# Kernel optimization log

Measured on AMD Instinct MI355X. Metric: run time of the kernel, lower is better.

The kernel has to match this reference:

```python
import jax, jax.numpy as jnp
import numpy as np

N_NODES = 100000
N_EDGES = 1600000
F_IN = 512
HEADS = 8
C1 = 8            # hidden per head in conv1
N_CLASSES = 40
NEG_SLOPE = 0.2
EPS = 1e-16


def setup_inputs() -> dict:
    key = jax.random.key(0)
    ks = jax.random.split(key, 12)
    x = jax.random.normal(ks[0], (N_NODES, F_IN), dtype=jnp.float32)
    # edges with src != dst (PyG SuperGAT removes then re-adds self-loops)
    src = jax.random.randint(ks[1], (N_EDGES,), 0, N_NODES)
    off = jax.random.randint(ks[2], (N_EDGES,), 1, N_NODES)
    dst = (src + off) % N_NODES
    edge_index = jnp.stack([src, dst]).astype(jnp.int64)
    def glorot(k, shape):
        fan = shape[0] + shape[-1]
        return jax.random.uniform(k, shape, jnp.float32, -1.0, 1.0) * np.sqrt(6.0 / fan)
    W1 = glorot(ks[3], (F_IN, HEADS * C1))
    att_l1 = glorot(ks[4], (HEADS, C1))
    att_r1 = glorot(ks[5], (HEADS, C1))
    b1 = jnp.zeros((HEADS * C1,), jnp.float32)
    W2 = glorot(ks[6], (HEADS * C1, HEADS * N_CLASSES))
    att_l2 = glorot(ks[7], (HEADS, N_CLASSES))
    att_r2 = glorot(ks[8], (HEADS, N_CLASSES))
    b2 = jnp.zeros((N_CLASSES,), jnp.float32)
    return {"x": x, "edge_index": edge_index, "W1": W1, "att_l1": att_l1,
            "att_r1": att_r1, "b1": b1, "W2": W2, "att_l2": att_l2,
            "att_r2": att_r2, "b2": b2}


def supergat_conv(x, edge_index, W, att_l, att_r, bias, concat):
    """SuperGATConv with attention_type='MX', eval mode (no dropout)."""
    N = x.shape[0]
    H, C = att_l.shape
    xw = (x @ W).reshape(N, H, C)
    loops = jnp.arange(N)
    src = jnp.concatenate([edge_index[0], loops])  # j (source)
    dst = jnp.concatenate([edge_index[1], loops])  # i (target)
    x_j = xw[src]                                   # [E,H,C]
    x_i = xw[dst]                                   # [E,H,C]
    # MX attention: GO score gated by sigmoid of DP logits
    logits = jnp.einsum('ehc,ehc->eh', x_i, x_j)
    alpha = jnp.einsum('ehc,hc->eh', x_j, att_l) + jnp.einsum('ehc,hc->eh', x_i, att_r)
    alpha = alpha * jax.nn.sigmoid(logits)
    alpha = jax.nn.leaky_relu(alpha, NEG_SLOPE)
    # segment softmax over incoming edges of each destination node
    amax = jax.ops.segment_max(alpha, dst, num_segments=N)
    e = jnp.exp(alpha - amax[dst])
    denom = jax.ops.segment_sum(e, dst, num_segments=N)
    a = e / (denom[dst] + EPS)
    out = jax.ops.segment_sum(x_j * a[..., None], dst, num_segments=N)  # [N,H,C]
    out = out.reshape(N, H * C) if concat else out.mean(axis=1)
    return out + bias


def reference(x, edge_index, W1, att_l1, att_r1, b1, W2, att_l2, att_r2, b2):
    # eval mode: F.dropout(p=0.6) is identity, att_loss is 0
    h = jax.nn.elu(supergat_conv(x, edge_index, W1, att_l1, att_r1, b1, concat=True))
    out = supergat_conv(h, edge_index, W2, att_l2, att_r2, b2, concat=False)
    att_loss = jnp.float32(0.0)
    return jax.nn.log_softmax(out, axis=-1), att_loss
```

## Files before the change

### kernel.cpp

```cpp
#include <hip/hip_runtime.h>
#include <cstdint>

#define N_NODES 100000
#define N_EDGES 1600000
#define SCAN_NB 196

typedef short bf16x8 __attribute__((ext_vector_type(8)));
typedef float f32x4 __attribute__((ext_vector_type(4)));
typedef float f32x2 __attribute__((ext_vector_type(2)));

__device__ __forceinline__ uint16_t f2bf(float f) {
    uint32_t b = __float_as_uint(f);
    return (uint16_t)((b + 0x7fffu + ((b >> 16) & 1u)) >> 16);
}
__device__ __forceinline__ float bfval(uint16_t u) {
    return __uint_as_float(((uint32_t)u) << 16);
}
__device__ __forceinline__ float blo(uint32_t u) { return __uint_as_float(u << 16); }
__device__ __forceinline__ float bhi(uint32_t u) { return __uint_as_float(u & 0xffff0000u); }

__device__ __forceinline__ float fast_rcp(float x) { return __builtin_amdgcn_rcpf(x); }

__global__ void cvt_w1(const float* __restrict__ W1, uint16_t* __restrict__ whi,
                       uint16_t* __restrict__ wlo) {
    int gid = blockIdx.x * 256 + threadIdx.x;
    int c = gid & 63, kg = gid >> 6;
    uint32_t dh[4], dl[4];
    #pragma unroll
    for (int t = 0; t < 4; ++t) {
        float v0 = W1[(kg * 8 + 2 * t) * 64 + c];
        float v1 = W1[(kg * 8 + 2 * t + 1) * 64 + c];
        uint16_t h0 = f2bf(v0), h1 = f2bf(v1);
        uint16_t l0 = f2bf(v0 - bfval(h0)), l1 = f2bf(v1 - bfval(h1));
        dh[t] = h0 | ((uint32_t)h1 << 16);
        dl[t] = l0 | ((uint32_t)l1 << 16);
    }
    *(uint4*)(whi + (long)c * 512 + kg * 8) = make_uint4(dh[0], dh[1], dh[2], dh[3]);
    *(uint4*)(wlo + (long)c * 512 + kg * 8) = make_uint4(dl[0], dl[1], dl[2], dl[3]);
}

__global__ __launch_bounds__(256) void wvec_k(const float* __restrict__ W2,
        const float* __restrict__ attl, const float* __restrict__ attr,
        float* __restrict__ wl2, float* __restrict__ wr2) {
    int t = blockIdx.x * 256 + threadIdx.x;
    if (t >= 512) return;
    int h = t >> 6, k = t & 63;
    float sl = 0.f, sr = 0.f;
    #pragma unroll 8
    for (int c = 0; c < 40; ++c) {
        float w = W2[k * 320 + h * 40 + c];
        sl += w * attl[h * 40 + c];
        sr += w * attr[h * 40 + c];
    }
    wl2[t] = sl; wr2[t] = sr;
}

__global__ __launch_bounds__(512) void mcat_k(const float* __restrict__ W2,
        uint16_t* __restrict__ mhi, uint16_t* __restrict__ mlo) {
    __shared__ float Wh[64 * 40];
    int h = blockIdx.x;
    int tid = threadIdx.x;
    for (int t = tid; t < 2560; t += 512) {
        int k = t / 40, c = t % 40;
        Wh[k * 40 + c] = W2[k * 320 + h * 40 + c];
    }
    __syncthreads();
    #pragma unroll
    for (int r = 0; r < 8; ++r) {
        int o = r * 512 + tid;
        int kp = o >> 6, k = o & 63;
        float s = 0.f;
        #pragma unroll 8
        for (int c = 0; c < 40; ++c) s += Wh[k * 40 + c] * Wh[kp * 40 + c];
        uint16_t hi = f2bf(s);
        uint16_t lo = f2bf(s - bfval(hi));
        mhi[(h * 64 + kp) * 64 + k] = hi;
        mlo[(h * 64 + kp) * 64 + k] = lo;
    }
}

__global__ __launch_bounds__(256) void w2z_k(const float* __restrict__ W2,
        uint16_t* __restrict__ w2z) {
    int t = blockIdx.x * 256 + threadIdx.x;
    if (t >= 24576) return;
    int c = t >> 9, kap = t & 511;
    int h = kap >> 6, k = kap & 63;
    float v = (c < 40) ? W2[k * 320 + h * 40 + c] : 0.f;
    w2z[c * 512 + kap] = f2bf(v);
}

__global__ __launch_bounds__(512) void gemm1_mfma(const float* __restrict__ x,
        const uint16_t* __restrict__ w1hi, const uint16_t* __restrict__ w1lo,
        float* __restrict__ xw1, uint16_t* __restrict__ xw1b) {
    __shared__ __align__(16) char Ah[128 * 144];
    __shared__ __align__(16) char Al[128 * 144];
    __shared__ __align__(16) char Bh[64 * 144];
    __shared__ __align__(16) char Bl[64 * 144];
    int tid = threadIdx.x;
    int l = tid & 63, w = tid >> 6;
    long base = (long)blockIdx.x * 128;
    f32x4 acc[4];
    #pragma unroll
    for (int ct = 0; ct < 4; ++ct)
        #pragma unroll
        for (int j = 0; j < 4; ++j) acc[ct][j] = 0.f;

    for (int kb = 0; kb < 512; kb += 64) {
        __syncthreads();
        #pragma unroll
        for (int it = 0; it < 2; ++it) {
            int idx = tid + it * 512;
            int row = idx >> 3, kc = idx & 7;
            long r = base + row; if (r >= N_NODES) r = N_NODES - 1;
            const float4* p = (const float4*)(x + r * 512 + kb + kc * 8);
            float4 f0 = p[0], f1 = p[1];
            float v[8] = {f0.x, f0.y, f0.z, f0.w, f1.x, f1.y, f1.z, f1.w};
            uint32_t dh[4], dl[4];
            #pragma unroll
            for (int t = 0; t < 4; ++t) {
                uint16_t h0 = f2bf(v[2 * t]),     h1 = f2bf(v[2 * t + 1]);
                uint16_t l0 = f2bf(v[2 * t] - bfval(h0));
                uint16_t l1 = f2bf(v[2 * t + 1] - bfval(h1));
                dh[t] = h0 | ((uint32_t)h1 << 16);
                dl[t] = l0 | ((uint32_t)l1 << 16);
            }
            *(uint4*)(Ah + row * 144 + kc * 16) = make_uint4(dh[0], dh[1], dh[2], dh[3]);
            *(uint4*)(Al + row * 144 + kc * 16) = make_uint4(dl[0], dl[1], dl[2], dl[3]);
        }
        {
            int c = tid >> 3, kc = tid & 7;
            *(uint4*)(Bh + c * 144 + kc * 16) =
                *(const uint4*)(w1hi + (long)c * 512 + kb + kc * 8);
            *(uint4*)(Bl + c * 144 + kc * 16) =
                *(const uint4*)(w1lo + (long)c * 512 + kb + kc * 8);
        }
        __syncthreads();
        #pragma unroll
        for (int kk = 0; kk < 2; ++kk) {
            int aoff = (w * 16 + (l & 15)) * 144 + kk * 64 + (l >> 4) * 16;
            bf16x8 ah = *(const bf16x8*)(Ah + aoff);
            bf16x8 alo = *(const bf16x8*)(Al + aoff);
            #pragma unroll
            for (int ct = 0; ct < 4; ++ct) {
                int boff = (ct * 16 + (l & 15)) * 144 + kk * 64 + (l >> 4) * 16;
                bf16x8 bh = *(const bf16x8*)(Bh + boff);
                bf16x8 bl = *(const bf16x8*)(Bl + boff);
                acc[ct] = __builtin_amdgcn_mfma_f32_16x16x32_bf16(ah, bh, acc[ct], 0, 0, 0);
                acc[ct] = __builtin_amdgcn_mfma_f32_16x16x32_bf16(alo, bh, acc[ct], 0, 0, 0);
                acc[ct] = __builtin_amdgcn_mfma_f32_16x16x32_bf16(ah, bl, acc[ct], 0, 0, 0);
            }
        }
    }
    int nrow = w * 16 + (l >> 4) * 4;
    #pragma unroll
    for (int ct = 0; ct < 4; ++ct)
        #pragma unroll
        for (int j = 0; j < 4; ++j) {
            long node = base + nrow + j;
            if (node < N_NODES) {
                int col = ct * 16 + (l & 15);
                xw1[node * 64 + col] = acc[ct][j];
                xw1b[node * 64 + col] = f2bf(acc[ct][j]);
            }
        }
}

__global__ __launch_bounds__(512) void ygemm_mfma(const uint16_t* __restrict__ hjb,
        const uint16_t* __restrict__ mhi, const uint16_t* __restrict__ mlo,
        uint16_t* __restrict__ Y16) {
    __shared__ __align__(16) char Bh[256 * 144];
    __shared__ __align__(16) char Bl[256 * 144];
    int tid = threadIdx.x;
    int l = tid & 63, w = tid >> 6;
    int half = blockIdx.x & 1;
    long base = (long)(blockIdx.x >> 1) * 128;
    #pragma unroll
    for (int it = 0; it < 4; ++it) {
        int idx = tid + it * 512;
        int c = idx >> 3, kc = idx & 7;
        *(uint4*)(Bh + c * 144 + kc * 16) =
            *(const uint4*)(mhi + (long)(half * 256 + c) * 64 + kc * 8);
        *(uint4*)(Bl + c * 144 + kc * 16) =
            *(const uint4*)(mlo + (long)(half * 256 + c) * 64 + kc * 8);
    }
    long n0 = base + w * 16 + (l & 15);
    long nld = n0 < N_NODES ? n0 : N_NODES - 1;
    bf16x8 a[2];
    #pragma unroll
    for (int kk = 0; kk < 2; ++kk)
        a[kk] = *(const bf16x8*)(hjb + nld * 64 + kk * 32 + (l >> 4) * 8);
    __syncthreads();
    f32x4 acc[16];
    #pragma unroll
    for (int ct = 0; ct < 16; ++ct)
        #pragma unroll
        for (int j = 0; j < 4; ++j) acc[ct][j] = 0.f;
    #pragma unroll
    for (int ct = 0; ct < 16; ++ct) {
        #pragma unroll
        for (int kk = 0; kk < 2; ++kk) {
            bf16x8 bh = *(const bf16x8*)(Bh + (ct * 16 + (l & 15)) * 144 + kk * 64 + (l >> 4) * 16);
            bf16x8 bl = *(const bf16x8*)(Bl + (ct * 16 + (l & 15)) * 144 + kk * 64 + (l >> 4) * 16);
            acc[ct] = __builtin_amdgcn_mfma_f32_16x16x32_bf16(bh, a[kk], acc[ct], 0, 0, 0);
            acc[ct] = __builtin_amdgcn_mfma_f32_16x16x32_bf16(bl, a[kk], acc[ct], 0, 0, 0);
        }
    }
    if (n0 < N_NODES) {
        uint32_t* Yd = (uint32_t*)Y16;
        #pragma unroll
        for (int ct = 0; ct < 16; ++ct) {
            int kp = half * 256 + ct * 16 + (l >> 4) * 4;
            uint32_t d0 = f2bf(acc[ct][0]) | ((uint32_t)f2bf(acc[ct][1]) << 16);
            uint32_t d1 = f2bf(acc[ct][2]) | ((uint32_t)f2bf(acc[ct][3]) << 16);
            Yd[n0 * 256 + (kp >> 1)]     = d0;
            Yd[n0 * 256 + (kp >> 1) + 1] = d1;
        }
    }
}

__global__ void hist_k(const int* __restrict__ dst, int* __restrict__ deg) {
    int e = blockIdx.x * blockDim.x + threadIdx.x;
    if (e < N_EDGES) atomicAdd(&deg[dst[e]], 1);
}

__global__ __launch_bounds__(512) void scan_a(const int* __restrict__ deg,
        int* __restrict__ offs, int* __restrict__ btot) {
    __shared__ int sh[512];
    int t = threadIdx.x;
    int g = blockIdx.x * 512 + t;
    int v = (g < N_NODES) ? deg[g] : 0;
    sh[t] = v;
    __syncthreads();
    #pragma unroll
    for (int o = 1; o < 512; o <<= 1) {
        int add = (t >= o) ? sh[t - o] : 0;
        __syncthreads();
        sh[t] += add;
        __syncthreads();
    }
    if (g < N_NODES) offs[g] = sh[t] - v;
    if (t == 511) btot[blockIdx.x] = sh[511];
}

__global__ __launch_bounds__(256) void scan_b(int* __restrict__ btot) {
    __shared__ int sh[256];
    int t = threadIdx.x;
    int v = (t < SCAN_NB) ? btot[t] : 0;
    sh[t] = v;
    __syncthreads();
    #pragma unroll
    for (int o = 1; o < 256; o <<= 1) {
        int add = (t >= o) ? sh[t - o] : 0;
        __syncthreads();
        sh[t] += add;
        __syncthreads();
    }
    if (t < SCAN_NB) btot[t] = sh[t] - v;
}

__global__ __launch_bounds__(512) void scan_c(int* __restrict__ offs,
        const int* __restrict__ btot, int* __restrict__ cursor) {
    int g = blockIdx.x * 512 + threadIdx.x;
    if (g < N_NODES) {
        int o = offs[g] + btot[blockIdx.x];
        offs[g] = o;
        cursor[g] = o;
    }
}

__global__ void scatter_k(const int* __restrict__ src, const int* __restrict__ dst,
        int* __restrict__ cursor, int* __restrict__ csr8) {
    int e = blockIdx.x * blockDim.x + threadIdx.x;
    if (e < N_EDGES) {
        int pos = atomicAdd(&cursor[dst[e]], 1);
        csr8[pos] = src[e] << 3;
    }
}

__global__ __launch_bounds__(256) void conv1_node(const float* __restrict__ xw,
        const uint16_t* __restrict__ xwb,
        const int* __restrict__ offs, const int* __restrict__ deg,
        const int* __restrict__ csr8, const float* __restrict__ att_l,
        const float* __restrict__ att_r, const float* __restrict__ b1,
        float* __restrict__ hout, uint16_t* __restrict__ hjb) {
    int wid = (blockIdx.x * blockDim.x + threadIdx.x) >> 6;
    if (wid >= N_NODES) return;
    int i = wid;
    int lane = threadIdx.x & 63;
    int g = lane >> 3, h = lane & 7;
    const float4* rowi = (const float4*)(xw + (long)i * 64 + h * 8);
    float4 xi0 = rowi[0], xi1 = rowi[1];
    f32x2 xip[4] = {{xi0.x, xi0.y}, {xi0.z, xi0.w}, {xi1.x, xi1.y}, {xi1.z, xi1.w}};
    const float4* alp4 = (const float4*)(att_l + h * 8);
    float4 t0 = alp4[0], t1 = alp4[1];
    f32x2 atlp[4] = {{t0.x, t0.y}, {t0.z, t0.w}, {t1.x, t1.y}, {t1.z, t1.w}};
    const float4* arp4 = (const float4*)(att_r + h * 8);
    float4 u0 = arp4[0], u1 = arp4[1];
    f32x2 atrp[4] = {{u0.x, u0.y}, {u0.z, u0.w}, {u1.x, u1.y}, {u1.z, u1.w}};
    f32x2 prp = xip[0] * atrp[0];
    prp += xip[1] * atrp[1];
    prp += xip[2] * atrp[2];
    prp += xip[3] * atrp[3];
    float pr = prp.x + prp.y;
    f32x2 accp[4] = {{0.f,0.f},{0.f,0.f},{0.f,0.f},{0.f,0.f}};
    float den = 0.f;

#define C1_EDGE(XJP) do { \
    f32x2 qdp = xip[0] * (XJP)[0]; \
    qdp += xip[1] * (XJP)[1]; \
    qdp += xip[2] * (XJP)[2]; \
    qdp += xip[3] * (XJP)[3]; \
    f32x2 qlp = (XJP)[0] * atlp[0]; \
    qlp += (XJP)[1] * atlp[1]; \
    qlp += (XJP)[2] * atlp[2]; \
    qlp += (XJP)[3] * atlp[3]; \
    float qd = qdp.x + qdp.y, ql = qlp.x + qlp.y; \
    float a = (ql + pr) * fast_rcp(1.0f + __expf(-qd)); \
    a = fmaxf(a, 0.2f * a); \
    float e = __expf(a); \
    den += e; \
    f32x2 ev = {e, e}; \
    accp[0] += ev * (XJP)[0]; \
    accp[1] += ev * (XJP)[1]; \
    accp[2] += ev * (XJP)[2]; \
    accp[3] += ev * (XJP)[3]; \
} while (0)

    if (g == 0) C1_EDGE(xip);
    int off = offs[i], dg = deg[i];
    int k = g;
    for (; k + 8 < dg; k += 16) {
        int j0 = csr8[off + k], j1 = csr8[off + k + 8];
        uint4 q0 = *(const uint4*)(xwb + (long)j0 * 8 + h * 8);
        uint4 q1 = *(const uint4*)(xwb + (long)j1 * 8 + h * 8);
        f32x2 ap[4] = {{blo(q0.x), bhi(q0.x)}, {blo(q0.y), bhi(q0.y)},
                       {blo(q0.z), bhi(q0.z)}, {blo(q0.w), bhi(q0.w)}};
        f32x2 bp[4] = {{blo(q1.x), bhi(q1.x)}, {blo(q1.y), bhi(q1.y)},
                       {blo(q1.z), bhi(q1.z)}, {blo(q1.w), bhi(q1.w)}};
        C1_EDGE(ap);
        C1_EDGE(bp);
    }
    if (k < dg) {
        int j0 = csr8[off + k];
        uint4 q0 = *(const uint4*)(xwb + (long)j0 * 8 + h * 8);
        f32x2 ap[4] = {{blo(q0.x), bhi(q0.x)}, {blo(q0.y), bhi(q0.y)},
                       {blo(q0.z), bhi(q0.z)}, {blo(q0.w), bhi(q0.w)}};
        C1_EDGE(ap);
    }
#undef C1_EDGE

    float acc[8] = {accp[0].x, accp[0].y, accp[1].x, accp[1].y,
                    accp[2].x, accp[2].y, accp[3].x, accp[3].y};
    #pragma unroll
    for (int o = 8; o <= 32; o <<= 1) {
        #pragma unroll
        for (int t = 0; t < 8; ++t) acc[t] += __shfl_xor(acc[t], o);
        den += __shfl_xor(den, o);
    }
    if (g == 0) {
        float inv = fast_rcp(den + 1e-16f);
        const float4* bp4 = (const float4*)(b1 + h * 8);
        float4 c0 = bp4[0], c1 = bp4[1];
        float4 o0, o1;
        float v;
        v = acc[0]*inv + c0.x; o0.x = v > 0.f ? v : __expf(v) - 1.0f;
        v = acc[1]*inv + c0.y; o0.y = v > 0.f ? v : __expf(v) - 1.0f;
        v = acc[2]*inv + c0.z; o0.z = v > 0.f ? v : __expf(v) - 1.0f;
        v = acc[3]*inv + c0.w; o0.w = v > 0.f ? v : __expf(v) - 1.0f;
        v = acc[4]*inv + c1.x; o1.x = v > 0.f ? v : __expf(v) - 1.0f;
        v = acc[5]*inv + c1.y; o1.y = v > 0.f ? v : __expf(v) - 1.0f;
        v = acc[6]*inv + c1.z; o1.z = v > 0.f ? v : __expf(v) - 1.0f;
        v = acc[7]*inv + c1.w; o1.w = v > 0.f ? v : __expf(v) - 1.0f;
        float4* po = (float4*)(hout + (long)i * 64 + h * 8);
        po[0] = o0; po[1] = o1;
        uint32_t d0 = f2bf(o0.x) | ((uint32_t)f2bf(o0.y) << 16);
        uint32_t d1 = f2bf(o0.z) | ((uint32_t)f2bf(o0.w) << 16);
        uint32_t d2 = f2bf(o1.x) | ((uint32_t)f2bf(o1.y) << 16);
        uint32_t d3 = f2bf(o1.z) | ((uint32_t)f2bf(o1.w) << 16);
        *(uint4*)(hjb + (long)i * 64 + h * 8) = make_uint4(d0, d1, d2, d3);
    }
}

__global__ __launch_bounds__(256) void node_att2h(const float* __restrict__ hbuf,
        const float* __restrict__ wl2, const float* __restrict__ wr2,
        float* __restrict__ al, float* __restrict__ ar) {
    __shared__ float lw[512], lr[512];
    int tid = threadIdx.x;
    for (int t = tid; t < 512; t += 256) { lw[t] = wl2[t]; lr[t] = wr2[t]; }
    __syncthreads();
    int i = blockIdx.x * 256 + tid;
    if (i >= N_NODES) return;
    const float4* row = (const float4*)(hbuf + (long)i * 64);
    float sl[8] = {0,0,0,0,0,0,0,0}, sr[8] = {0,0,0,0,0,0,0,0};
    #pragma unroll
    for (int d4 = 0; d4 < 16; ++d4) {
        float4 v = row[d4];
        #pragma unroll
        for (int hh = 0; hh < 8; ++hh) {
            const float4 wv = *(const float4*)(lw + hh * 64 + d4 * 4);
            const float4 rv = *(const float4*)(lr + hh * 64 + d4 * 4);
            sl[hh] += v.x*wv.x + v.y*wv.y + v.z*wv.z + v.w*wv.w;
            sr[hh] += v.x*rv.x + v.y*rv.y + v.z*rv.z + v.w*rv.w;
        }
    }
    #pragma unroll
    for (int hh = 0; hh < 8; ++hh) {
        al[i * 8 + hh] = sl[hh];
        ar[i * 8 + hh] = sr[hh];
    }
}

__global__ __launch_bounds__(256) void conv2_node(const uint16_t* __restrict__ hjb16,
        const int* __restrict__ offs, const int* __restrict__ deg,
        const int* __restrict__ csr8, const float* __restrict__ al,
        const float* __restrict__ ar, uint32_t* __restrict__ Yd) {
    int wid = (blockIdx.x * 256 + threadIdx.x) >> 6;
    if (wid >= N_NODES) return;
    int i = wid;
    int lane = threadIdx.x & 63;
    int half = lane >> 5;
    int lam = lane & 7, r2 = (lane >> 3) & 3;
    const uint32_t* hjd = (const uint32_t*)hjb16;
    unsigned ydw = (unsigned)i * 256u + (unsigned)lam * 32u + (unsigned)r2 * 8u;

    f32x2 y[8];
    {
        uint4 a = *(const uint4*)(Yd + ydw);
        uint4 b = *(const uint4*)(Yd + ydw + 4);
        uint32_t d[8] = {a.x, a.y, a.z, a.w, b.x, b.y, b.z, b.w};
        #pragma unroll
        for (int t = 0; t < 8; ++t) y[t] = (f32x2){blo(d[t]), bhi(d[t])};
    }
    float ari = ar[i * 8 + lam];
    f32x2 agg[8];
    #pragma unroll
    for (int t = 0; t < 8; ++t) agg[t] = (f32x2){0.f, 0.f};
    float den = 0.f;
    int off = offs[i], dg = deg[i];

    auto CORE = [&](const uint32_t* D, float alv, bool valid) {
        f32x2 h[8];
        #pragma unroll
        for (int t = 0; t < 8; ++t) h[t] = (f32x2){blo(D[t]), bhi(D[t])};
        f32x2 pp = y[0] * h[0];
        #pragma unroll
        for (int t = 1; t < 8; ++t) pp += y[t] * h[t];
        float pd = pp.x + pp.y;
        pd += __shfl_xor(pd, 8);
        pd += __shfl_xor(pd, 16);
        float a = (alv + ari) * fast_rcp(1.0f + __expf(-pd));
        a = fmaxf(a, 0.2f * a);
        float e = __expf(a);
        e = valid ? e : 0.f;
        den += e;
        f32x2 ev = {e, e};
        #pragma unroll
        for (int t = 0; t < 8; ++t) agg[t] += ev * h[t];
    };
    auto IDX = [&](int S) -> int {
        int e = half + 2 * S;
        int p = off + e;
        p = p < N_EDGES ? p : 0;
        int j = csr8[p];
        return e < dg ? j : 0;
    };
    auto FETCH = [&](int j, uint32_t* D, float& A) {
        const uint32_t* r = hjd + (unsigned)j * 4u + (unsigned)r2 * 8u;
        uint4 a = *(const uint4*)(r);
        uint4 b = *(const uint4*)(r + 4);
        D[0] = a.x; D[1] = a.y; D[2] = a.z; D[3] = a.w;
        D[4] = b.x; D[5] = b.y; D[6] = b.z; D[7] = b.w;
        A = al[j + lam];
    };

    {
        uint32_t DS[8]; float AS;
        FETCH(i * 8, DS, AS);
        CORE(DS, AS, half == 0);
    }

    int nT = (dg + 1) >> 1;
    uint32_t D0[8], D1[8]; float A0, A1;
    { int j = IDX(0); FETCH(j, D0, A0); }
    { int j = IDX(1); FETCH(j, D1, A1); }
    int s = 0;
    while (s + 2 <= nT) {
        int j2 = IDX(s + 2);
        CORE(D0, A0, half + 2 * s < dg);
        FETCH(j2, D0, A0);
        int j3 = IDX(s + 3);
        CORE(D1, A1, half + 2 * (s + 1) < dg);
        FETCH(j3, D1, A1);
        s += 2;
    }
    if (s < nT)     CORE(D0, A0, half + 2 * s < dg);
    if (s + 1 < nT) CORE(D1, A1, half + 2 * (s + 1) < dg);

    den += __shfl_xor(den, 32);
    #pragma unroll
    for (int t = 0; t < 8; ++t) {
        agg[t].x += __shfl_xor(agg[t].x, 32);
        agg[t].y += __shfl_xor(agg[t].y, 32);
    }
    float inv = 0.125f * fast_rcp(den + 1e-16f);
    if (half == 0) {
        uint32_t zd[8];
        #pragma unroll
        for (int t = 0; t < 8; ++t) {
            float zx = agg[t].x * inv, zy = agg[t].y * inv;
            zd[t] = f2bf(zx) | ((uint32_t)f2bf(zy) << 16);
        }
        *(uint4*)(Yd + ydw)     = make_uint4(zd[0], zd[1], zd[2], zd[3]);
        *(uint4*)(Yd + ydw + 4) = make_uint4(zd[4], zd[5], zd[6], zd[7]);
    }
}

__global__ __launch_bounds__(512) void zgemm_mfma(const uint32_t* __restrict__ Zd,
        const uint16_t* __restrict__ w2z, const float* __restrict__ b2,
        float* __restrict__ out) {
    __shared__ __align__(16) uint16_t Bsm[48 * 520];
    int tid = threadIdx.x;
    int l = tid & 63, w = tid >> 6;
    long base = (long)blockIdx.x * 128;
    for (int q = tid; q < 3072; q += 512) {
        int c = q >> 6, k8 = (q & 63) * 8;
        *(uint4*)(Bsm + c * 520 + k8) = *(const uint4*)(w2z + c * 512 + k8);
    }
    if (blockIdx.x == 0 && tid == 0) out[(long)N_NODES * 40] = 0.0f;
    __syncthreads();
    long n0 = base + w * 16 + (l & 15);
    long nld = n0 < N_NODES ? n0 : N_NODES - 1;
    f32x4 acc[3];
    #pragma unroll
    for (int ct = 0; ct < 3; ++ct)
        #pragma unroll
        for (int j = 0; j < 4; ++j) acc[ct][j] = 0.f;
    #pragma unroll
    for (int kb = 0; kb < 16; ++kb) {
        bf16x8 a = *(const bf16x8*)(Zd + nld * 256 + kb * 16 + (l >> 4) * 4);
        #pragma unroll
        for (int ct = 0; ct < 3; ++ct) {
            bf16x8 b = *(const bf16x8*)(Bsm + (ct * 16 + (l & 15)) * 520 + kb * 32 + (l >> 4) * 8);
            acc[ct] = __builtin_amdgcn_mfma_f32_16x16x32_bf16(b, a, acc[ct], 0, 0, 0);
        }
    }
    float v[12];
    int cb0 = (l >> 4) * 4;
    #pragma unroll
    for (int ct = 0; ct < 3; ++ct)
        #pragma unroll
        for (int j = 0; j < 4; ++j) {
            int cb = ct * 16 + cb0 + j;
            v[ct * 4 + j] = (cb < 40) ? acc[ct][j] + b2[cb] : -1e30f;
        }
    float mx = v[0];
    #pragma unroll
    for (int t = 1; t < 12; ++t) mx = fmaxf(mx, v[t]);
    mx = fmaxf(mx, __shfl_xor(mx, 16));
    mx = fmaxf(mx, __shfl_xor(mx, 32));
    float sm = 0.f;
    #pragma unroll
    for (int t = 0; t < 12; ++t) sm += (v[t] > -1e29f) ? __expf(v[t] - mx) : 0.f;
    sm += __shfl_xor(sm, 16);
    sm += __shfl_xor(sm, 32);
    float lse = mx + __logf(sm);
    if (n0 < N_NODES) {
        #pragma unroll
        for (int ct = 0; ct < 3; ++ct)
            #pragma unroll
            for (int j = 0; j < 4; ++j) {
                int cb = ct * 16 + cb0 + j;
                if (cb < 40) out[n0 * 40 + cb] = v[ct * 4 + j] - lse;
            }
    }
}

extern "C" void kernel_launch(void* const* d_in, const int* in_sizes, int n_in,
                              void* d_out, int out_size, void* d_ws, size_t ws_size,
                              hipStream_t stream) {
    const float* x      = (const float*)d_in[0];
    const int*   ei     = (const int*)d_in[1];
    const float* W1     = (const float*)d_in[2];
    const float* att_l1 = (const float*)d_in[3];
    const float* att_r1 = (const float*)d_in[4];
    const float* b1     = (const float*)d_in[5];
    const float* W2     = (const float*)d_in[6];
    const float* att_l2 = (const float*)d_in[7];
    const float* att_r2 = (const float*)d_in[8];
    const float* b2     = (const float*)d_in[9];
    const int* src = ei;
    const int* dst = ei + N_EDGES;
    float* out = (float*)d_out;

    char* ws = (char*)d_ws;
    uint16_t* Y      = (uint16_t*)(ws + 0);
    float*    xw1    = (float*)(ws + 0);
    float*    hbuf   = (float*)(ws + 25600000);
    uint16_t* xw1b   = (uint16_t*)(ws + 51200000);
    uint16_t* hjb    = (uint16_t*)(ws + 102400000);
    float*    al     = (float*)(ws + 115200000);
    float*    ar     = (float*)(ws + 118400000);
    int*      deg    = (int*)(ws + 121600000);
    int*      offs   = (int*)(ws + 122000000);
    int*      cursor = (int*)(ws + 122400000);
    int*      btot   = (int*)(ws + 122800000);
    int*      csr8   = (int*)(ws + 122801024);
    uint16_t* w1hi   = (uint16_t*)(ws + 129201024);
    uint16_t* w1lo   = (uint16_t*)(ws + 129266560);
    uint16_t* mhi    = (uint16_t*)(ws + 129332096);
    uint16_t* mlo    = (uint16_t*)(ws + 129397632);
    uint16_t* w2z    = (uint16_t*)(ws + 129463168);
    float*    wl2    = (float*)(ws + 129512320);
    float*    wr2    = (float*)(ws + 129514368);

    hipMemsetAsync(deg, 0, (size_t)N_NODES * 4, stream);

    cvt_w1<<<16, 256, 0, stream>>>(W1, w1hi, w1lo);
    wvec_k<<<2, 256, 0, stream>>>(W2, att_l2, att_r2, wl2, wr2);
    mcat_k<<<8, 512, 0, stream>>>(W2, mhi, mlo);
    w2z_k<<<96, 256, 0, stream>>>(W2, w2z);

    hist_k<<<6250, 256, 0, stream>>>(dst, deg);
    scan_a<<<SCAN_NB, 512, 0, stream>>>(deg, offs, btot);
    scan_b<<<1, 256, 0, stream>>>(btot);
    scan_c<<<SCAN_NB, 512, 0, stream>>>(offs, btot, cursor);
    scatter_k<<<6250, 256, 0, stream>>>(src, dst, cursor, csr8);

    gemm1_mfma<<<782, 512, 0, stream>>>(x, w1hi, w1lo, xw1, xw1b);
    conv1_node<<<25000, 256, 0, stream>>>(xw1, xw1b, offs, deg, csr8,
                                          att_l1, att_r1, b1, hbuf, hjb);
    node_att2h<<<391, 256, 0, stream>>>(hbuf, wl2, wr2, al, ar);

    ygemm_mfma<<<1564, 512, 0, stream>>>(hjb, mhi, mlo, Y);

    conv2_node<<<25000, 256, 0, stream>>>(hjb, offs, deg, csr8, al, ar, (uint32_t*)Y);

    zgemm_mfma<<<782, 512, 0, stream>>>((const uint32_t*)Y, w2z, b2, out);
}
```

Baseline: 565.3 us.

## Merge weight-prep kernels, fuse conv2 attention logits into conv1, retune conv2 prefetch

The four small weight-preprocessing kernels become one multi-role launch. The per-node layer-2 attention projections (al/ar) are now computed inside conv1_node from the in-register ELU output, which drops the fp32 hbuf write and the separate node_att2h pass. conv2_node gets a deeper, unguarded software-pipelined prefetch loop with the odd tail edge handled separately, and uses ds_swizzle instead of shfl for the partial reductions. This cuts launches and memory traffic at the cost of more complex tail logic and extra work across all lanes in conv1.

```diff
diff --git a/kernel.cpp b/kernel.cpp
--- a/kernel.cpp
+++ b/kernel.cpp
@@ -20,73 +20,75 @@
 __device__ __forceinline__ float bhi(uint32_t u) { return __uint_as_float(u & 0xffff0000u); }
 
 __device__ __forceinline__ float fast_rcp(float x) { return __builtin_amdgcn_rcpf(x); }
-
-__global__ void cvt_w1(const float* __restrict__ W1, uint16_t* __restrict__ whi,
-                       uint16_t* __restrict__ wlo) {
-    int gid = blockIdx.x * 256 + threadIdx.x;
-    int c = gid & 63, kg = gid >> 6;
-    uint32_t dh[4], dl[4];
-    #pragma unroll
-    for (int t = 0; t < 4; ++t) {
-        float v0 = W1[(kg * 8 + 2 * t) * 64 + c];
-        float v1 = W1[(kg * 8 + 2 * t + 1) * 64 + c];
-        uint16_t h0 = f2bf(v0), h1 = f2bf(v1);
-        uint16_t l0 = f2bf(v0 - bfval(h0)), l1 = f2bf(v1 - bfval(h1));
-        dh[t] = h0 | ((uint32_t)h1 << 16);
-        dl[t] = l0 | ((uint32_t)l1 << 16);
-    }
-    *(uint4*)(whi + (long)c * 512 + kg * 8) = make_uint4(dh[0], dh[1], dh[2], dh[3]);
-    *(uint4*)(wlo + (long)c * 512 + kg * 8) = make_uint4(dl[0], dl[1], dl[2], dl[3]);
-}
-
-__global__ __launch_bounds__(256) void wvec_k(const float* __restrict__ W2,
-        const float* __restrict__ attl, const float* __restrict__ attr,
-        float* __restrict__ wl2, float* __restrict__ wr2) {
-    int t = blockIdx.x * 256 + threadIdx.x;
-    if (t >= 512) return;
-    int h = t >> 6, k = t & 63;
-    float sl = 0.f, sr = 0.f;
-    #pragma unroll 8
-    for (int c = 0; c < 40; ++c) {
-        float w = W2[k * 320 + h * 40 + c];
-        sl += w * attl[h * 40 + c];
-        sr += w * attr[h * 40 + c];
-    }
-    wl2[t] = sl; wr2[t] = sr;
-}
-
-__global__ __launch_bounds__(512) void mcat_k(const float* __restrict__ W2,
-        uint16_t* __restrict__ mhi, uint16_t* __restrict__ mlo) {
+__device__ __forceinline__ float swz_xadd8(float x) {
+    int s = __builtin_amdgcn_ds_swizzle(__float_as_int(x), 0x201F);
+    return x + __int_as_float(s);
+}
+__device__ __forceinline__ float swz_xadd16(float x) {
+    int s = __builtin_amdgcn_ds_swizzle(__float_as_int(x), 0x401F);
+    return x + __int_as_float(s);
+}
+
+__global__ __launch_bounds__(512) void prep_k(const float* __restrict__ W1,
+        const float* __restrict__ W2, const float* __restrict__ attl,
+        const float* __restrict__ attr,
+        uint16_t* __restrict__ w1hi, uint16_t* __restrict__ w1lo,
+        float* __restrict__ wl2, float* __restrict__ wr2,
+        uint16_t* __restrict__ w2z, uint16_t* __restrict__ mhi,
+        uint16_t* __restrict__ mlo) {
     __shared__ float Wh[64 * 40];
-    int h = blockIdx.x;
-    int tid = threadIdx.x;
-    for (int t = tid; t < 2560; t += 512) {
-        int k = t / 40, c = t % 40;
-        Wh[k * 40 + c] = W2[k * 320 + h * 40 + c];
-    }
-    __syncthreads();
-    #pragma unroll
-    for (int r = 0; r < 8; ++r) {
-        int o = r * 512 + tid;
-        int kp = o >> 6, k = o & 63;
-        float s = 0.f;
+    int b = blockIdx.x, tid = threadIdx.x;
+    if (b < 8) {
+        int gid = b * 512 + tid;
+        int c = gid & 63, kg = gid >> 6;
+        uint32_t dh[4], dl[4];
+        #pragma unroll
+        for (int t = 0; t < 4; ++t) {
+            float v0 = W1[(kg * 8 + 2 * t) * 64 + c];
+            float v1 = W1[(kg * 8 + 2 * t + 1) * 64 + c];
+            uint16_t h0 = f2bf(v0), h1 = f2bf(v1);
+            uint16_t l0 = f2bf(v0 - bfval(h0)), l1 = f2bf(v1 - bfval(h1));
+            dh[t] = h0 | ((uint32_t)h1 << 16);
+            dl[t] = l0 | ((uint32_t)l1 << 16);
+        }
+        *(uint4*)(w1hi + (long)c * 512 + kg * 8) = make_uint4(dh[0], dh[1], dh[2], dh[3]);
+        *(uint4*)(w1lo + (long)c * 512 + kg * 8) = make_uint4(dl[0], dl[1], dl[2], dl[3]);
+    } else if (b == 8) {
+        int h = tid >> 6, k = tid & 63;
+        float sl = 0.f, sr = 0.f;
         #pragma unroll 8
-        for (int c = 0; c < 40; ++c) s += Wh[k * 40 + c] * Wh[kp * 40 + c];
-        uint16_t hi = f2bf(s);
-        uint16_t lo = f2bf(s - bfval(hi));
-        mhi[(h * 64 + kp) * 64 + k] = hi;
-        mlo[(h * 64 + kp) * 64 + k] = lo;
-    }
-}
-
-__global__ __launch_bounds__(256) void w2z_k(const float* __restrict__ W2,
-        uint16_t* __restrict__ w2z) {
-    int t = blockIdx.x * 256 + threadIdx.x;
-    if (t >= 24576) return;
-    int c = t >> 9, kap = t & 511;
-    int h = kap >> 6, k = kap & 63;
-    float v = (c < 40) ? W2[k * 320 + h * 40 + c] : 0.f;
-    w2z[c * 512 + kap] = f2bf(v);
+        for (int c = 0; c < 40; ++c) {
+            float w = W2[k * 320 + h * 40 + c];
+            sl += w * attl[h * 40 + c];
+            sr += w * attr[h * 40 + c];
+        }
+        wl2[tid] = sl; wr2[tid] = sr;
+    } else if (b < 57) {
+        int t = (b - 9) * 512 + tid;
+        int c = t >> 9, kap = t & 511;
+        int h = kap >> 6, k = kap & 63;
+        float v = (c < 40) ? W2[k * 320 + h * 40 + c] : 0.f;
+        w2z[c * 512 + kap] = f2bf(v);
+    } else {
+        int h = b - 57;
+        for (int t = tid; t < 2560; t += 512) {
+            int k = t / 40, c = t % 40;
+            Wh[k * 40 + c] = W2[k * 320 + h * 40 + c];
+        }
+        __syncthreads();
+        #pragma unroll
+        for (int r = 0; r < 8; ++r) {
+            int o = r * 512 + tid;
+            int kp = o >> 6, k = o & 63;
+            float s = 0.f;
+            #pragma unroll 8
+            for (int c = 0; c < 40; ++c) s += Wh[k * 40 + c] * Wh[kp * 40 + c];
+            uint16_t hi = f2bf(s);
+            uint16_t lo = f2bf(s - bfval(hi));
+            mhi[(h * 64 + kp) * 64 + k] = hi;
+            mlo[(h * 64 + kp) * 64 + k] = lo;
+        }
+    }
 }
 
 __global__ __launch_bounds__(512) void gemm1_mfma(const float* __restrict__ x,
@@ -282,7 +284,8 @@
         const int* __restrict__ offs, const int* __restrict__ deg,
         const int* __restrict__ csr8, const float* __restrict__ att_l,
         const float* __restrict__ att_r, const float* __restrict__ b1,
-        float* __restrict__ hout, uint16_t* __restrict__ hjb) {
+        const float* __restrict__ wl2, const float* __restrict__ wr2,
+        uint16_t* __restrict__ hjb, float* __restrict__ al, float* __restrict__ ar) {
     int wid = (blockIdx.x * blockDim.x + threadIdx.x) >> 6;
     if (wid >= N_NODES) return;
     int i = wid;
@@ -357,56 +360,41 @@
         for (int t = 0; t < 8; ++t) acc[t] += __shfl_xor(acc[t], o);
         den += __shfl_xor(den, o);
     }
+    float inv = fast_rcp(den + 1e-16f);
+    const float4* bp4 = (const float4*)(b1 + h * 8);
+    float4 c0 = bp4[0], c1 = bp4[1];
+    float bias[8] = {c0.x, c0.y, c0.z, c0.w, c1.x, c1.y, c1.z, c1.w};
+    float ov[8];
+    #pragma unroll
+    for (int t = 0; t < 8; ++t) {
+        float v = acc[t] * inv + bias[t];
+        ov[t] = v > 0.f ? v : __expf(v) - 1.0f;
+    }
     if (g == 0) {
-        float inv = fast_rcp(den + 1e-16f);
-        const float4* bp4 = (const float4*)(b1 + h * 8);
-        float4 c0 = bp4[0], c1 = bp4[1];
-        float4 o0, o1;
-        float v;
-        v = acc[0]*inv + c0.x; o0.x = v > 0.f ? v : __expf(v) - 1.0f;
-        v = acc[1]*inv + c0.y; o0.y = v > 0.f ? v : __expf(v) - 1.0f;
-        v = acc[2]*inv + c0.z; o0.z = v > 0.f ? v : __expf(v) - 1.0f;
-        v = acc[3]*inv + c0.w; o0.w = v > 0.f ? v : __expf(v) - 1.0f;
-        v = acc[4]*inv + c1.x; o1.x = v > 0.f ? v : __expf(v) - 1.0f;
-        v = acc[5]*inv + c1.y; o1.y = v > 0.f ? v : __expf(v) - 1.0f;
-        v = acc[6]*inv + c1.z; o1.z = v > 0.f ? v : __expf(v) - 1.0f;
-        v = acc[7]*inv + c1.w; o1.w = v > 0.f ? v : __expf(v) - 1.0f;
-        float4* po = (float4*)(hout + (long)i * 64 + h * 8);
-        po[0] = o0; po[1] = o1;
-        uint32_t d0 = f2bf(o0.x) | ((uint32_t)f2bf(o0.y) << 16);
-        uint32_t d1 = f2bf(o0.z) | ((uint32_t)f2bf(o0.w) << 16);
-        uint32_t d2 = f2bf(o1.x) | ((uint32_t)f2bf(o1.y) << 16);
-        uint32_t d3 = f2bf(o1.z) | ((uint32_t)f2bf(o1.w) << 16);
+        uint32_t d0 = f2bf(ov[0]) | ((uint32_t)f2bf(ov[1]) << 16);
+        uint32_t d1 = f2bf(ov[2]) | ((uint32_t)f2bf(ov[3]) << 16);
+        uint32_t d2 = f2bf(ov[4]) | ((uint32_t)f2bf(ov[5]) << 16);
+        uint32_t d3 = f2bf(ov[6]) | ((uint32_t)f2bf(ov[7]) << 16);
         *(uint4*)(hjb + (long)i * 64 + h * 8) = make_uint4(d0, d1, d2, d3);
     }
-}
-
-__global__ __launch_bounds__(256) void node_att2h(const float* __restrict__ hbuf,
-        const float* __restrict__ wl2, const float* __restrict__ wr2,
-        float* __restrict__ al, float* __restrict__ ar) {
-    __shared__ float lw[512], lr[512];
-    int tid = threadIdx.x;
-    for (int t = tid; t < 512; t += 256) { lw[t] = wl2[t]; lr[t] = wr2[t]; }
-    __syncthreads();
-    int i = blockIdx.x * 256 + tid;
-    if (i >= N_NODES) return;
-    const float4* row = (const float4*)(hbuf + (long)i * 64);
-    float sl[8] = {0,0,0,0,0,0,0,0}, sr[8] = {0,0,0,0,0,0,0,0};
-    #pragma unroll
-    for (int d4 = 0; d4 < 16; ++d4) {
-        float4 v = row[d4];
-        #pragma unroll
-        for (int hh = 0; hh < 8; ++hh) {
-            const float4 wv = *(const float4*)(lw + hh * 64 + d4 * 4);
-            const float4 rv = *(const float4*)(lr + hh * 64 + d4 * 4);
-            sl[hh] += v.x*wv.x + v.y*wv.y + v.z*wv.z + v.w*wv.w;
-            sr[hh] += v.x*rv.x + v.y*rv.y + v.z*rv.z + v.w*rv.w;
-        }
-    }
-    #pragma unroll
-    for (int hh = 0; hh < 8; ++hh) {
-        al[i * 8 + hh] = sl[hh];
-        ar[i * 8 + hh] = sr[hh];
+    {
+        const float4* wlp = (const float4*)(wl2 + g * 64 + h * 8);
+        float4 w0 = wlp[0], w1 = wlp[1];
+        const float4* wrp = (const float4*)(wr2 + g * 64 + h * 8);
+        float4 r0 = wrp[0], r1 = wrp[1];
+        float sl = ov[0]*w0.x + ov[1]*w0.y + ov[2]*w0.z + ov[3]*w0.w
+                 + ov[4]*w1.x + ov[5]*w1.y + ov[6]*w1.z + ov[7]*w1.w;
+        float sr = ov[0]*r0.x + ov[1]*r0.y + ov[2]*r0.z + ov[3]*r0.w
+                 + ov[4]*r1.x + ov[5]*r1.y + ov[6]*r1.z + ov[7]*r1.w;
+        #pragma unroll
+        for (int o = 1; o <= 4; o <<= 1) {
+            sl += __shfl_xor(sl, o);
+            sr += __shfl_xor(sr, o);
+        }
+        if (h == 0) {
+            al[i * 8 + g] = sl;
+            ar[i * 8 + g] = sr;
+        }
     }
 }
 
@@ -420,7 +408,8 @@
     int lane = threadIdx.x & 63;
     int half = lane >> 5;
     int lam = lane & 7, r2 = (lane >> 3) & 3;
-    const uint32_t* hjd = (const uint32_t*)hjb16;
+    const uint4* hj4 = (const uint4*)hjb16;
+    int r22 = r2 * 2;
     unsigned ydw = (unsigned)i * 256u + (unsigned)lam * 32u + (unsigned)r2 * 8u;
 
     f32x2 y[8];
@@ -438,7 +427,7 @@
     float den = 0.f;
     int off = offs[i], dg = deg[i];
 
-    auto CORE = [&](const uint32_t* D, float alv, bool valid) {
+    auto CORE = [&](const uint32_t* D, float alv) {
         f32x2 h[8];
         #pragma unroll
         for (int t = 0; t < 8; ++t) h[t] = (f32x2){blo(D[t]), bhi(D[t])};
@@ -446,8 +435,26 @@
         #pragma unroll
         for (int t = 1; t < 8; ++t) pp += y[t] * h[t];
         float pd = pp.x + pp.y;
-        pd += __shfl_xor(pd, 8);
-        pd += __shfl_xor(pd, 16);
+        pd = swz_xadd8(pd);
+        pd = swz_xadd16(pd);
+        float a = (alv + ari) * fast_rcp(1.0f + __expf(-pd));
+        a = fmaxf(a, 0.2f * a);
+        float e = __expf(a);
+        den += e;
+        f32x2 ev = {e, e};
+        #pragma unroll
+        for (int t = 0; t < 8; ++t) agg[t] += ev * h[t];
+    };
+    auto COREG = [&](const uint32_t* D, float alv, bool valid) {
+        f32x2 h[8];
+        #pragma unroll
+        for (int t = 0; t < 8; ++t) h[t] = (f32x2){blo(D[t]), bhi(D[t])};
+        f32x2 pp = y[0] * h[0];
+        #pragma unroll
+        for (int t = 1; t < 8; ++t) pp += y[t] * h[t];
+        float pd = pp.x + pp.y;
+        pd = swz_xadd8(pd);
+        pd = swz_xadd16(pd);
         float a = (alv + ari) * fast_rcp(1.0f + __expf(-pd));
         a = fmaxf(a, 0.2f * a);
         float e = __expf(a);
@@ -457,17 +464,11 @@
         #pragma unroll
         for (int t = 0; t < 8; ++t) agg[t] += ev * h[t];
     };
-    auto IDX = [&](int S) -> int {
-        int e = half + 2 * S;
-        int p = off + e;
-        p = p < N_EDGES ? p : 0;
+    auto PF = [&](int p, uint32_t* D, float& A) {
+        p = p < N_EDGES ? p : N_EDGES - 1;
         int j = csr8[p];
-        return e < dg ? j : 0;
-    };
-    auto FETCH = [&](int j, uint32_t* D, float& A) {
-        const uint32_t* r = hjd + (unsigned)j * 4u + (unsigned)r2 * 8u;
-        uint4 a = *(const uint4*)(r);
-        uint4 b = *(const uint4*)(r + 4);
+        const uint4* r = hj4 + (unsigned)j + r22;
+        uint4 a = r[0], b = r[1];
         D[0] = a.x; D[1] = a.y; D[2] = a.z; D[3] = a.w;
         D[4] = b.x; D[5] = b.y; D[6] = b.z; D[7] = b.w;
         A = al[j + lam];
@@ -475,26 +476,42 @@
 
     {
         uint32_t DS[8]; float AS;
-        FETCH(i * 8, DS, AS);
-        CORE(DS, AS, half == 0);
-    }
-
-    int nT = (dg + 1) >> 1;
-    uint32_t D0[8], D1[8]; float A0, A1;
-    { int j = IDX(0); FETCH(j, D0, A0); }
-    { int j = IDX(1); FETCH(j, D1, A1); }
+        const uint4* r = hj4 + (unsigned)i * 8u + r22;
+        uint4 a = r[0], b = r[1];
+        DS[0] = a.x; DS[1] = a.y; DS[2] = a.z; DS[3] = a.w;
+        DS[4] = b.x; DS[5] = b.y; DS[6] = b.z; DS[7] = b.w;
+        AS = al[i * 8 + lam];
+        COREG(DS, AS, half == 0);
+    }
+
+    int nP = dg >> 1;
+    int base = off + half;
+    uint32_t R0[8], R1[8], T0[8], T1[8];
+    float A0, A1, B0, B1;
+    PF(base,     R0, A0);
+    PF(base + 2, R1, A1);
     int s = 0;
-    while (s + 2 <= nT) {
-        int j2 = IDX(s + 2);
-        CORE(D0, A0, half + 2 * s < dg);
-        FETCH(j2, D0, A0);
-        int j3 = IDX(s + 3);
-        CORE(D1, A1, half + 2 * (s + 1) < dg);
-        FETCH(j3, D1, A1);
-        s += 2;
-    }
-    if (s < nT)     CORE(D0, A0, half + 2 * s < dg);
-    if (s + 1 < nT) CORE(D1, A1, half + 2 * (s + 1) < dg);
+    while (s + 4 <= nP) {
+        PF(base + 2*s + 4,  T0, B0); CORE(R0, A0);
+        PF(base + 2*s + 6,  T1, B1); CORE(R1, A1);
+        PF(base + 2*s + 8,  R0, A0); CORE(T0, B0);
+        PF(base + 2*s + 10, R1, A1); CORE(T1, B1);
+        s += 4;
+    }
+    int rem = nP - s;
+    if (rem >= 2) {
+        PF(base + 2*s + 4, T0, B0);
+        CORE(R0, A0);
+        CORE(R1, A1);
+        if (rem == 3) CORE(T0, B0);
+    } else if (rem == 1) {
+        CORE(R0, A0);
+    }
+    if (dg & 1) {
+        uint32_t RT[8]; float AT;
+        PF(off + dg - 1, RT, AT);
+        COREG(RT, AT, half == 0);
+    }
 
     den += __shfl_xor(den, 32);
     #pragma unroll
@@ -595,8 +612,7 @@
     char* ws = (char*)d_ws;
     uint16_t* Y      = (uint16_t*)(ws + 0);
     float*    xw1    = (float*)(ws + 0);
-    float*    hbuf   = (float*)(ws + 25600000);
-    uint16_t* xw1b   = (uint16_t*)(ws + 51200000);
+    uint16_t* xw1b   = (uint16_t*)(ws + 25600000);
     uint16_t* hjb    = (uint16_t*)(ws + 102400000);
     float*    al     = (float*)(ws + 115200000);
     float*    ar     = (float*)(ws + 118400000);
@@ -615,10 +631,8 @@
 
     hipMemsetAsync(deg, 0, (size_t)N_NODES * 4, stream);
 
-    cvt_w1<<<16, 256, 0, stream>>>(W1, w1hi, w1lo);
-    wvec_k<<<2, 256, 0, stream>>>(W2, att_l2, att_r2, wl2, wr2);
-    mcat_k<<<8, 512, 0, stream>>>(W2, mhi, mlo);
-    w2z_k<<<96, 256, 0, stream>>>(W2, w2z);
+    prep_k<<<65, 512, 0, stream>>>(W1, W2, att_l2, att_r2,
+                                   w1hi, w1lo, wl2, wr2, w2z, mhi, mlo);
 
     hist_k<<<6250, 256, 0, stream>>>(dst, deg);
     scan_a<<<SCAN_NB, 512, 0, stream>>>(deg, offs, btot);
@@ -628,8 +642,8 @@
 
     gemm1_mfma<<<782, 512, 0, stream>>>(x, w1hi, w1lo, xw1, xw1b);
     conv1_node<<<25000, 256, 0, stream>>>(xw1, xw1b, offs, deg, csr8,
-                                          att_l1, att_r1, b1, hbuf, hjb);
-    node_att2h<<<391, 256, 0, stream>>>(hbuf, wl2, wr2, al, ar);
+                                          att_l1, att_r1, b1, wl2, wr2,
+                                          hjb, al, ar);
 
     ygemm_mfma<<<1564, 512, 0, stream>>>(hjb, mhi, mlo, Y);
 
```

New measurement: 561.6 us. No clear change (-0.6%).
